# Optimization experiments

Hardware: AMD Instinct MI355X
Metric: run time of the kernel (lower is better)

## Reference

```python
import jax, jax.numpy as jnp
import numpy as np

TAU = 0.07          # softmax temperature
THR = 0.3           # Jaccard similarity threshold for positive pairs
EPS_NORM = 1e-12    # F.normalize eps


def setup_inputs() -> dict:
    key = jax.random.key(0)
    k1, k2, k3 = jax.random.split(key, 3)
    N, D, A = 4096, 128, 512
    z1 = jax.random.normal(k1, (N, D), dtype=jnp.float32)
    z2 = jax.random.normal(k2, (N, D), dtype=jnp.float32)
    labels = jax.random.randint(k3, (N, A), 0, 2).astype(jnp.int32)
    return {"z1": z1, "z2": z2, "labels": labels}


def _l2_normalize(x):
    n = jnp.linalg.norm(x, axis=-1, keepdims=True)
    return x / jnp.maximum(n, EPS_NORM)


def reference(z1, z2, labels):
    # Implements the N > 1000 (chunked) branch of SupConLoss.forward,
    # vectorized over all anchors at once (chunking is just tiling; math identical).
    N = z1.shape[0]
    idx = jnp.arange(N)

    z1n = _l2_normalize(z1)                       # (N, D)
    z2n = _l2_normalize(z2)                       # (N, D)
    z_all = jnp.concatenate([z1n, z2n], axis=0)   # (2N, D)

    # Jaccard label similarity -> positive-pair mask
    lab = labels.astype(jnp.float32)              # (N, A)
    inter = lab @ lab.T                           # (N, N)
    s = lab.sum(axis=1, keepdims=True)            # (N, 1)
    union = s + s.T - inter
    jaccard = inter / (union + 1e-8)
    pos_label = jaccard >= THR                    # (N, N) bool

    # pos mask over 2N columns: label-positives in both halves,
    # augmented view [j, N+j] forced True, self column [j, j] forced False.
    pos_mask = jnp.concatenate([pos_label, pos_label], axis=1)  # (N, 2N)
    pos_mask = pos_mask.at[idx, N + idx].set(True)
    pos_mask = pos_mask.at[idx, idx].set(False)

    # similarity of z1 anchors against all 2N embeddings
    sim = (z1n @ z_all.T) / TAU                   # (N, 2N)
    sim = sim - jax.lax.stop_gradient(sim.max(axis=1, keepdims=True))
    exp_sim = jnp.exp(sim)

    # denominator excludes the self column [j, j]
    denom = exp_sim.sum(axis=1, keepdims=True) - exp_sim[idx, idx][:, None]
    log_prob = sim - jnp.log(denom + 1e-8)

    num_pos = jnp.maximum(pos_mask.sum(axis=1), 1)
    loss_per_sample = -jnp.where(pos_mask, log_prob, 0.0).sum(axis=1) / num_pos
    return loss_per_sample.sum() / N
```

## Files before the change

kernel.cpp:

```cpp
#include <hip/hip_runtime.h>
#include <math.h>

#define N_ROWS 4096
#define DIM    128
#define A_LAB  512
#define INV_TAU 14.285714285714286f

typedef __attribute__((ext_vector_type(8))) short short8;
typedef __attribute__((ext_vector_type(4))) float f32x4;
typedef __attribute__((ext_vector_type(4))) int i32x4;
typedef __attribute__((ext_vector_type(16))) int i32x16;


__device__ __forceinline__ unsigned short f2bf(float f) {
  unsigned int u = __builtin_bit_cast(unsigned int, f);
  u += 0x7fffu + ((u >> 16) & 1u);
  return (unsigned short)(u >> 16);
}

__device__ __forceinline__ void gl_lds16(const void* g, void* l) {
  __builtin_amdgcn_global_load_lds(
      (const __attribute__((address_space(1))) unsigned int*)g,
      (__attribute__((address_space(3))) unsigned int*)l, 16, 0, 0);
}

__global__ __launch_bounds__(256) void k_norm_pack(
    const float* __restrict__ z1, const float* __restrict__ z2,
    const int* __restrict__ labels,
    unsigned int* __restrict__ zbf, uint2* __restrict__ labs8,
    int* __restrict__ s, float* __restrict__ out)
{
  if (blockIdx.x == 0 && threadIdx.x == 0) out[0] = 0.0f;
  const int wave = threadIdx.x >> 6, lane = threadIdx.x & 63;
  const int r = blockIdx.x * 4 + wave;
  const float* src = (r < N_ROWS) ? (z1 + (size_t)r * DIM)
                                  : (z2 + (size_t)(r - N_ROWS) * DIM);
  float2 x = ((const float2*)src)[lane];
  float ss = x.x * x.x + x.y * x.y;
  #pragma unroll
  for (int off = 32; off > 0; off >>= 1) ss += __shfl_xor(ss, off);
  const float inv = 1.0f / fmaxf(sqrtf(ss), 1e-12f);
  const unsigned int lo = f2bf(x.x * inv);
  const unsigned int hi = f2bf(x.y * inv);
  {
    const int U  = lane >> 2;
    const int Up = U ^ (r & 15);
    zbf[(size_t)r * 64 + Up * 4 + (lane & 3)] = (hi << 16) | lo;
  }

  if (r < N_ROWS) {
    const int4* lp = (const int4*)(labels + (size_t)r * A_LAB);
    const int4 a = lp[2 * lane], b = lp[2 * lane + 1];
    const unsigned int w0 = (unsigned int)(a.x != 0)       | ((unsigned int)(a.y != 0) << 8)
                          | ((unsigned int)(a.z != 0) << 16) | ((unsigned int)(a.w != 0) << 24);
    const unsigned int w1 = (unsigned int)(b.x != 0)       | ((unsigned int)(b.y != 0) << 8)
                          | ((unsigned int)(b.z != 0) << 16) | ((unsigned int)(b.w != 0) << 24);
    uint2 v; v.x = w0; v.y = w1;
    const int Ul  = lane >> 1;
    const int cc  = Ul >> 3, uu = Ul & 7;
    const int Ulp = (cc << 3) | (uu ^ (r & 7));
    labs8[(size_t)r * 64 + Ulp * 2 + (lane & 1)] = v;
    int cnt = __popc(w0) + __popc(w1);
    #pragma unroll
    for (int off = 32; off > 0; off >>= 1) cnt += __shfl_xor(cnt, off);
    if (lane == 0) s[r] = cnt;
  }
}

__global__ __launch_bounds__(256, 2) void k_jac(
    const unsigned char* __restrict__ labs8, const int* __restrict__ s,
    unsigned int* __restrict__ pm)
{
  __shared__ uint4 lds[4096];
  const int tid = threadIdx.x;
  const int ibase = blockIdx.x * 128, jbase = blockIdx.y * 128;
  const int wave = tid >> 6, lane = tid & 63;
  const int wrow = (wave >> 1) * 64, wcol = (wave & 1) * 64;
  const int col = lane & 31, h = lane >> 5;

  const int s3i = 3 * s[ibase + wrow + lane];
  const int s3j = 3 * s[jbase + wcol + lane];

  #pragma unroll
  for (int it = 0; it < 4; ++it) {
    const int g = wave * 256 + it * 64 + lane;
    const int r = g >> 3, u = g & 7;
    gl_lds16(labs8 + (((size_t)(ibase + r)) << 9) + u * 16,
             &lds[wave * 256 + it * 64]);
    gl_lds16(labs8 + (((size_t)(jbase + r)) << 9) + u * 16,
             &lds[1024 + wave * 256 + it * 64]);
  }
  __syncthreads();

  i32x16 acc[2][2];
  #pragma unroll
  for (int rt = 0; rt < 2; ++rt)
    #pragma unroll
    for (int nt = 0; nt < 2; ++nt)
      #pragma unroll
      for (int e = 0; e < 16; ++e) acc[rt][nt][e] = 0;

  for (int ck = 0; ck < 4; ++ck) {
    const int cur = (ck & 1) * 2048;
    if (ck < 3) {
      const int nxt = ((ck + 1) & 1) * 2048;
      #pragma unroll
      for (int it = 0; it < 4; ++it) {
        const int g = wave * 256 + it * 64 + lane;
        const int r = g >> 3, u = g & 7;
        const size_t go = (size_t)(ck + 1) * 128 + u * 16;
        gl_lds16(labs8 + (((size_t)(ibase + r)) << 9) + go,
                 &lds[nxt + wave * 256 + it * 64]);
        gl_lds16(labs8 + (((size_t)(jbase + r)) << 9) + go,
                 &lds[nxt + 1024 + wave * 256 + it * 64]);
      }
    }
    #pragma unroll
    for (int ks = 0; ks < 4; ++ks) {
      const int u = ks * 2 + h;
      i32x4 a[2], b[2];
      #pragma unroll
      for (int rt = 0; rt < 2; ++rt) {
        const int m = wrow + rt * 32 + col;
        a[rt] = *(const i32x4*)&lds[cur + m * 8 + (u ^ (m & 7))];
      }
      #pragma unroll
      for (int nt = 0; nt < 2; ++nt) {
        const int m = wcol + nt * 32 + col;
        b[nt] = *(const i32x4*)&lds[cur + 1024 + m * 8 + (u ^ (m & 7))];
      }
      #pragma unroll
      for (int rt = 0; rt < 2; ++rt)
        #pragma unroll
        for (int nt = 0; nt < 2; ++nt)
          acc[rt][nt] = __builtin_amdgcn_mfma_i32_32x32x32_i8(a[rt], b[nt], acc[rt][nt], 0, 0, 0);
    }
    if (ck < 3) __syncthreads();
  }

  #pragma unroll
  for (int rt = 0; rt < 2; ++rt)
    #pragma unroll
    for (int nt = 0; nt < 2; ++nt) {
      const int w = (jbase + wcol + nt * 32) >> 5;
      const int sj = __shfl(s3j, nt * 32 + col);
      #pragma unroll
      for (int reg = 0; reg < 16; ++reg) {
        const int r0 = (reg & 3) + 8 * (reg >> 2);
        const int si = __shfl(s3i, rt * 32 + r0 + 4 * h);
        const bool pred = 13 * acc[rt][nt][reg] >= si + sj;
        const unsigned long long bal = __ballot(pred);
        const int i0 = ibase + wrow + rt * 32 + r0;
        if (lane == 0)      pm[(size_t)i0 * 128 + w]       = (unsigned int)bal;
        else if (lane == 1) pm[(size_t)(i0 + 4) * 128 + w] = (unsigned int)(bal >> 32);
      }
    }
}

__global__ __launch_bounds__(256, 2) void k_main(
    const unsigned short* __restrict__ zbf, const unsigned int* __restrict__ pm,
    float* __restrict__ part)
{
  __shared__ unsigned short lds[2 * 128 * 128];
  uint4* sU = (uint4*)lds;
  const int tid = threadIdx.x;
  const int abase = blockIdx.x * 128;
  const int cbase = blockIdx.y * 128;
  const int wave = tid >> 6, lane = tid & 63;

  {
    const char* gz = (const char*)zbf;
    #pragma unroll
    for (int it = 0; it < 8; ++it) {
      const int g = wave * 512 + it * 64 + lane;
      const int r = g >> 4, u = g & 15;
      gl_lds16(gz + (size_t)(abase + r) * 256 + u * 16, &sU[wave * 512 + it * 64]);
      gl_lds16(gz + (size_t)(cbase + r) * 256 + u * 16, &sU[2048 + wave * 512 + it * 64]);
    }
  }
  __syncthreads();

  const int col = lane & 15, quad = lane >> 4;
  const int wrow = wave * 32;
  const uint4* sAu = sU;
  const uint4* sBu = sU + 2048;

  short8 afr[2][4];
  #pragma unroll
  for (int rt = 0; rt < 2; ++rt)
    #pragma unroll
    for (int kf = 0; kf < 4; ++kf) {
      const int r = wrow + rt * 16 + col;
      const int u = kf * 4 + quad;
      afr[rt][kf] = *(const short8*)&sAu[r * 16 + (u ^ (r & 15))];
    }

  f32x4 acc[2][8];
  #pragma unroll
  for (int rt = 0; rt < 2; ++rt)
    #pragma unroll
    for (int nt = 0; nt < 8; ++nt) acc[rt][nt] = (f32x4){0, 0, 0, 0};

  #pragma unroll
  for (int nt = 0; nt < 8; ++nt) {
    short8 bfr[4];
    #pragma unroll
    for (int kf = 0; kf < 4; ++kf) {
      const int r = nt * 16 + col;
      const int u = kf * 4 + quad;
      bfr[kf] = *(const short8*)&sBu[r * 16 + (u ^ (r & 15))];
    }
    #pragma unroll
    for (int rt = 0; rt < 2; ++rt)
      #pragma unroll
      for (int kf = 0; kf < 4; ++kf)
        acc[rt][nt] = __builtin_amdgcn_mfma_f32_16x16x32_bf16(
            afr[rt][kf], bfr[kf], acc[rt][nt], 0, 0, 0);
  }

  const bool left = (cbase < N_ROWS);
  const int cw0 = (cbase & (N_ROWS - 1)) >> 5;
  float lacc[2][4], Sacc[2][4], Pcnt[2][4];
  #pragma unroll
  for (int rt = 0; rt < 2; ++rt)
    #pragma unroll
    for (int reg = 0; reg < 4; ++reg) { lacc[rt][reg] = 0; Sacc[rt][reg] = 0; Pcnt[rt][reg] = 0; }

  #pragma unroll
  for (int rt = 0; rt < 2; ++rt) {
    unsigned int pw[4][4];
    #pragma unroll
    for (int reg = 0; reg < 4; ++reg) {
      const int i = abase + wrow + rt * 16 + quad * 4 + reg;
      #pragma unroll
      for (int w = 0; w < 4; ++w) pw[reg][w] = pm[(size_t)i * 128 + cw0 + w];
    }
    #pragma unroll
    for (int nt = 0; nt < 8; ++nt) {
      const int j = cbase + nt * 16 + col;
      const int jc = j & (N_ROWS - 1);
      const int bitpos = jc & 31;
      const int w = nt >> 1;
      #pragma unroll
      for (int reg = 0; reg < 4; ++reg) {
        const int i = abase + wrow + rt * 16 + quad * 4 + reg;
        const float d = acc[rt][nt][reg];
        const bool bit = (pw[reg][w] >> bitpos) & 1;
        const bool self = left && (j == i);
        const bool pos = left ? (bit && !self) : (bit || (jc == i));
        const float e = __expf((d - 1.0f) * INV_TAU);
        if (!self) lacc[rt][reg] += e;
        if (pos) { Sacc[rt][reg] += d; Pcnt[rt][reg] += 1.0f; }
      }
    }
  }

  #pragma unroll
  for (int rt = 0; rt < 2; ++rt)
    #pragma unroll
    for (int reg = 0; reg < 4; ++reg) {
      float l = lacc[rt][reg], S = Sacc[rt][reg], P = Pcnt[rt][reg];
      #pragma unroll
      for (int m = 1; m < 16; m <<= 1) {
        l += __shfl_xor(l, m);
        S += __shfl_xor(S, m);
        P += __shfl_xor(P, m);
      }
      if (col == 0) {
        const int i = abase + wrow + rt * 16 + quad * 4 + reg;
        float* base = part + (size_t)blockIdx.y * 3 * 4096;
        base[i] = l;
        base[4096 + i] = S;
        base[8192 + i] = P;
      }
    }
}

__global__ __launch_bounds__(128) void k_loss(
    const float* __restrict__ part, float* __restrict__ out)
{
  const int a = blockIdx.x * 128 + threadIdx.x;
  float l = 0.0f, S = 0.0f, P = 0.0f;
  #pragma unroll 8
  for (int by = 0; by < 64; ++by) {
    const float* b = part + (size_t)by * 3 * 4096;
    l += b[a];
    S += b[4096 + a];
    P += b[8192 + a];
  }
  const float np = fmaxf(P, 1.0f);
  float v = INV_TAU + logf(l + 1e-8f) - (S * INV_TAU) / np;
  #pragma unroll
  for (int off = 32; off > 0; off >>= 1) v += __shfl_xor(v, off);
  __shared__ float ws2[2];
  const int wave = threadIdx.x >> 6, lane = threadIdx.x & 63;
  if (lane == 0) ws2[wave] = v;
  __syncthreads();
  if (threadIdx.x == 0) atomicAdd(out, (ws2[0] + ws2[1]) * (1.0f / (float)N_ROWS));
}

extern "C" void kernel_launch(void* const* d_in, const int* in_sizes, int n_in,
                              void* d_out, int out_size, void* d_ws, size_t ws_size,
                              hipStream_t stream) {
  const float* z1 = (const float*)d_in[0];
  const float* z2 = (const float*)d_in[1];
  const int* labels = (const int*)d_in[2];
  float* out = (float*)d_out;
  char* ws = (char*)d_ws;

  unsigned int* zbf    = (unsigned int*)(ws);
  uint2* labs8         = (uint2*)(ws + 2097152);
  int* s               = (int*)(ws + 4194304);
  unsigned int* pm     = (unsigned int*)(ws + 4210688);
  float* part          = (float*)(ws + 6307840);

  hipLaunchKernelGGL(k_norm_pack, dim3(2048), dim3(256), 0, stream,
                     z1, z2, labels, zbf, labs8, s, out);
  hipLaunchKernelGGL(k_jac, dim3(32, 32), dim3(256), 0, stream,
                     (const unsigned char*)labs8, s, pm);
  hipLaunchKernelGGL(k_main, dim3(32, 64), dim3(256), 0, stream,
                     (const unsigned short*)zbf, pm, part);
  hipLaunchKernelGGL(k_loss, dim3(32), dim3(128), 0, stream, part, out);
}
```

Before: 128.3 us.

## Fuse Jaccard mask and similarity kernels, keep positive mask in LDS

Merges the Jaccard mask kernel and the similarity/softmax kernel into one kernel per 128x128 tile. The positive-pair bitmask now lives in shared memory instead of a global round trip, and each block handles both the z1 and z2 column halves in sequence, reloading the B tile between them. Per-block partial sums are combined with float atomics into a single buffer zeroed in the pack kernel, so the final loss kernel no longer loops over 64 partial slices. This removes one launch and the global mask traffic, at the cost of longer blocks, extra barriers, atomic contention, and nondeterministic summation order.

```diff
diff --git a/kernel.cpp b/kernel.cpp
--- a/kernel.cpp
+++ b/kernel.cpp
@@ -28,9 +28,13 @@
     const float* __restrict__ z1, const float* __restrict__ z2,
     const int* __restrict__ labels,
     unsigned int* __restrict__ zbf, uint2* __restrict__ labs8,
-    int* __restrict__ s, float* __restrict__ out)
+    int* __restrict__ s, float* __restrict__ part, float* __restrict__ out)
 {
-  if (blockIdx.x == 0 && threadIdx.x == 0) out[0] = 0.0f;
+  {
+    const int idx = blockIdx.x * 256 + threadIdx.x;
+    if (idx < 3 * 4096) part[idx] = 0.0f;
+    if (idx == 0) out[0] = 0.0f;
+  }
   const int wave = threadIdx.x >> 6, lane = threadIdx.x & 63;
   const int r = blockIdx.x * 4 + wave;
   const float* src = (r < N_ROWS) ? (z1 + (size_t)r * DIM)
@@ -67,19 +71,21 @@
   }
 }
 
-__global__ __launch_bounds__(256, 2) void k_jac(
+__global__ __launch_bounds__(256, 2) void k_fused(
     const unsigned char* __restrict__ labs8, const int* __restrict__ s,
-    unsigned int* __restrict__ pm)
+    const unsigned short* __restrict__ zbf, float* __restrict__ part)
 {
   __shared__ uint4 lds[4096];
+  __shared__ unsigned int pmL[128 * 4];
   const int tid = threadIdx.x;
   const int ibase = blockIdx.x * 128, jbase = blockIdx.y * 128;
   const int wave = tid >> 6, lane = tid & 63;
-  const int wrow = (wave >> 1) * 64, wcol = (wave & 1) * 64;
-  const int col = lane & 31, h = lane >> 5;
-
-  const int s3i = 3 * s[ibase + wrow + lane];
-  const int s3j = 3 * s[jbase + wcol + lane];
+
+  const int jwr = (wave >> 1) * 64, jwc = (wave & 1) * 64;
+  const int col32 = lane & 31, h = lane >> 5;
+
+  const int s3i = 3 * s[ibase + jwr + lane];
+  const int s3j = 3 * s[jbase + jwc + lane];
 
   #pragma unroll
   for (int it = 0; it < 4; ++it) {
@@ -92,13 +98,13 @@
   }
   __syncthreads();
 
-  i32x16 acc[2][2];
+  i32x16 jacc[2][2];
   #pragma unroll
   for (int rt = 0; rt < 2; ++rt)
     #pragma unroll
     for (int nt = 0; nt < 2; ++nt)
       #pragma unroll
-      for (int e = 0; e < 16; ++e) acc[rt][nt][e] = 0;
+      for (int e = 0; e < 16; ++e) jacc[rt][nt][e] = 0;
 
   for (int ck = 0; ck < 4; ++ck) {
     const int cur = (ck & 1) * 2048;
@@ -121,138 +127,144 @@
       i32x4 a[2], b[2];
       #pragma unroll
       for (int rt = 0; rt < 2; ++rt) {
-        const int m = wrow + rt * 32 + col;
+        const int m = jwr + rt * 32 + col32;
         a[rt] = *(const i32x4*)&lds[cur + m * 8 + (u ^ (m & 7))];
       }
       #pragma unroll
       for (int nt = 0; nt < 2; ++nt) {
-        const int m = wcol + nt * 32 + col;
+        const int m = jwc + nt * 32 + col32;
         b[nt] = *(const i32x4*)&lds[cur + 1024 + m * 8 + (u ^ (m & 7))];
       }
       #pragma unroll
       for (int rt = 0; rt < 2; ++rt)
         #pragma unroll
         for (int nt = 0; nt < 2; ++nt)
-          acc[rt][nt] = __builtin_amdgcn_mfma_i32_32x32x32_i8(a[rt], b[nt], acc[rt][nt], 0, 0, 0);
+          jacc[rt][nt] = __builtin_amdgcn_mfma_i32_32x32x32_i8(a[rt], b[nt], jacc[rt][nt], 0, 0, 0);
     }
     if (ck < 3) __syncthreads();
   }
 
+  __syncthreads();
+
+  {
+    const char* gz = (const char*)zbf;
+    #pragma unroll
+    for (int it = 0; it < 8; ++it) {
+      const int g = wave * 512 + it * 64 + lane;
+      const int r = g >> 4, u = g & 15;
+      gl_lds16(gz + (size_t)(ibase + r) * 256 + u * 16, &lds[wave * 512 + it * 64]);
+      gl_lds16(gz + (size_t)(jbase + r) * 256 + u * 16, &lds[2048 + wave * 512 + it * 64]);
+    }
+  }
+
   #pragma unroll
   for (int rt = 0; rt < 2; ++rt)
     #pragma unroll
     for (int nt = 0; nt < 2; ++nt) {
-      const int w = (jbase + wcol + nt * 32) >> 5;
-      const int sj = __shfl(s3j, nt * 32 + col);
+      const int wl = (jwc >> 5) + nt;
+      const int sj = __shfl(s3j, nt * 32 + col32);
       #pragma unroll
       for (int reg = 0; reg < 16; ++reg) {
         const int r0 = (reg & 3) + 8 * (reg >> 2);
         const int si = __shfl(s3i, rt * 32 + r0 + 4 * h);
-        const bool pred = 13 * acc[rt][nt][reg] >= si + sj;
+        const bool pred = 13 * jacc[rt][nt][reg] >= si + sj;
         const unsigned long long bal = __ballot(pred);
-        const int i0 = ibase + wrow + rt * 32 + r0;
-        if (lane == 0)      pm[(size_t)i0 * 128 + w]       = (unsigned int)bal;
-        else if (lane == 1) pm[(size_t)(i0 + 4) * 128 + w] = (unsigned int)(bal >> 32);
-      }
-    }
-}
-
-__global__ __launch_bounds__(256, 2) void k_main(
-    const unsigned short* __restrict__ zbf, const unsigned int* __restrict__ pm,
-    float* __restrict__ part)
-{
-  __shared__ unsigned short lds[2 * 128 * 128];
-  uint4* sU = (uint4*)lds;
-  const int tid = threadIdx.x;
-  const int abase = blockIdx.x * 128;
-  const int cbase = blockIdx.y * 128;
-  const int wave = tid >> 6, lane = tid & 63;
-
-  {
-    const char* gz = (const char*)zbf;
-    #pragma unroll
-    for (int it = 0; it < 8; ++it) {
-      const int g = wave * 512 + it * 64 + lane;
-      const int r = g >> 4, u = g & 15;
-      gl_lds16(gz + (size_t)(abase + r) * 256 + u * 16, &sU[wave * 512 + it * 64]);
-      gl_lds16(gz + (size_t)(cbase + r) * 256 + u * 16, &sU[2048 + wave * 512 + it * 64]);
-    }
-  }
+        const int lr = jwr + rt * 32 + r0;
+        if (lane == 0)      pmL[lr * 4 + wl]       = (unsigned int)bal;
+        else if (lane == 1) pmL[(lr + 4) * 4 + wl] = (unsigned int)(bal >> 32);
+      }
+    }
+
   __syncthreads();
 
   const int col = lane & 15, quad = lane >> 4;
-  const int wrow = wave * 32;
-  const uint4* sAu = sU;
-  const uint4* sBu = sU + 2048;
+  const int swr = wave * 32;
+  const uint4* sAu = lds;
+  const uint4* sBu = lds + 2048;
 
   short8 afr[2][4];
   #pragma unroll
   for (int rt = 0; rt < 2; ++rt)
     #pragma unroll
     for (int kf = 0; kf < 4; ++kf) {
-      const int r = wrow + rt * 16 + col;
+      const int r = swr + rt * 16 + col;
       const int u = kf * 4 + quad;
       afr[rt][kf] = *(const short8*)&sAu[r * 16 + (u ^ (r & 15))];
     }
 
-  f32x4 acc[2][8];
-  #pragma unroll
-  for (int rt = 0; rt < 2; ++rt)
-    #pragma unroll
-    for (int nt = 0; nt < 8; ++nt) acc[rt][nt] = (f32x4){0, 0, 0, 0};
-
-  #pragma unroll
-  for (int nt = 0; nt < 8; ++nt) {
-    short8 bfr[4];
-    #pragma unroll
-    for (int kf = 0; kf < 4; ++kf) {
-      const int r = nt * 16 + col;
-      const int u = kf * 4 + quad;
-      bfr[kf] = *(const short8*)&sBu[r * 16 + (u ^ (r & 15))];
-    }
+  float lacc[2][4], Sacc[2][4], Pcnt[2][4];
+  #pragma unroll
+  for (int rt = 0; rt < 2; ++rt)
+    #pragma unroll
+    for (int reg = 0; reg < 4; ++reg) { lacc[rt][reg] = 0; Sacc[rt][reg] = 0; Pcnt[rt][reg] = 0; }
+
+  #pragma unroll
+  for (int half = 0; half < 2; ++half) {
+    f32x4 acc[2][8];
     #pragma unroll
     for (int rt = 0; rt < 2; ++rt)
       #pragma unroll
-      for (int kf = 0; kf < 4; ++kf)
-        acc[rt][nt] = __builtin_amdgcn_mfma_f32_16x16x32_bf16(
-            afr[rt][kf], bfr[kf], acc[rt][nt], 0, 0, 0);
-  }
-
-  const bool left = (cbase < N_ROWS);
-  const int cw0 = (cbase & (N_ROWS - 1)) >> 5;
-  float lacc[2][4], Sacc[2][4], Pcnt[2][4];
-  #pragma unroll
-  for (int rt = 0; rt < 2; ++rt)
-    #pragma unroll
-    for (int reg = 0; reg < 4; ++reg) { lacc[rt][reg] = 0; Sacc[rt][reg] = 0; Pcnt[rt][reg] = 0; }
-
-  #pragma unroll
-  for (int rt = 0; rt < 2; ++rt) {
-    unsigned int pw[4][4];
-    #pragma unroll
-    for (int reg = 0; reg < 4; ++reg) {
-      const int i = abase + wrow + rt * 16 + quad * 4 + reg;
-      #pragma unroll
-      for (int w = 0; w < 4; ++w) pw[reg][w] = pm[(size_t)i * 128 + cw0 + w];
-    }
+      for (int nt = 0; nt < 8; ++nt) acc[rt][nt] = (f32x4){0, 0, 0, 0};
+
     #pragma unroll
     for (int nt = 0; nt < 8; ++nt) {
-      const int j = cbase + nt * 16 + col;
-      const int jc = j & (N_ROWS - 1);
-      const int bitpos = jc & 31;
-      const int w = nt >> 1;
+      short8 bfr[4];
+      #pragma unroll
+      for (int kf = 0; kf < 4; ++kf) {
+        const int r = nt * 16 + col;
+        const int u = kf * 4 + quad;
+        bfr[kf] = *(const short8*)&sBu[r * 16 + (u ^ (r & 15))];
+      }
+      #pragma unroll
+      for (int rt = 0; rt < 2; ++rt)
+        #pragma unroll
+        for (int kf = 0; kf < 4; ++kf)
+          acc[rt][nt] = __builtin_amdgcn_mfma_f32_16x16x32_bf16(
+              afr[rt][kf], bfr[kf], acc[rt][nt], 0, 0, 0);
+    }
+
+    if (half == 0) {
+      __syncthreads();
+      const char* gz = (const char*)zbf;
+      #pragma unroll
+      for (int it = 0; it < 8; ++it) {
+        const int g = wave * 512 + it * 64 + lane;
+        const int r = g >> 4, u = g & 15;
+        gl_lds16(gz + (size_t)(N_ROWS + jbase + r) * 256 + u * 16,
+                 &lds[2048 + wave * 512 + it * 64]);
+      }
+    }
+
+    const bool left = (half == 0);
+    #pragma unroll
+    for (int rt = 0; rt < 2; ++rt) {
+      unsigned int pw[4][4];
       #pragma unroll
       for (int reg = 0; reg < 4; ++reg) {
-        const int i = abase + wrow + rt * 16 + quad * 4 + reg;
-        const float d = acc[rt][nt][reg];
-        const bool bit = (pw[reg][w] >> bitpos) & 1;
-        const bool self = left && (j == i);
-        const bool pos = left ? (bit && !self) : (bit || (jc == i));
-        const float e = __expf((d - 1.0f) * INV_TAU);
-        if (!self) lacc[rt][reg] += e;
-        if (pos) { Sacc[rt][reg] += d; Pcnt[rt][reg] += 1.0f; }
-      }
-    }
+        const int li = swr + rt * 16 + quad * 4 + reg;
+        #pragma unroll
+        for (int w = 0; w < 4; ++w) pw[reg][w] = pmL[li * 4 + w];
+      }
+      #pragma unroll
+      for (int nt = 0; nt < 8; ++nt) {
+        const int joff = nt * 16 + col;
+        const int jc = jbase + joff;
+        const int bitpos = joff & 31;
+        const int w = nt >> 1;
+        #pragma unroll
+        for (int reg = 0; reg < 4; ++reg) {
+          const int i = ibase + swr + rt * 16 + quad * 4 + reg;
+          const float d = acc[rt][nt][reg];
+          const bool bit = (pw[reg][w] >> bitpos) & 1;
+          const bool self = left && (jc == i);
+          const bool pos = left ? (bit && !self) : (bit || (jc == i));
+          const float e = __expf((d - 1.0f) * INV_TAU);
+          if (!self) lacc[rt][reg] += e;
+          if (pos) { Sacc[rt][reg] += d; Pcnt[rt][reg] += 1.0f; }
+        }
+      }
+    }
+    if (half == 0) __syncthreads();
   }
 
   #pragma unroll
@@ -267,11 +279,10 @@
         P += __shfl_xor(P, m);
       }
       if (col == 0) {
-        const int i = abase + wrow + rt * 16 + quad * 4 + reg;
-        float* base = part + (size_t)blockIdx.y * 3 * 4096;
-        base[i] = l;
-        base[4096 + i] = S;
-        base[8192 + i] = P;
+        const int i = ibase + swr + rt * 16 + quad * 4 + reg;
+        atomicAdd(&part[i], l);
+        atomicAdd(&part[4096 + i], S);
+        atomicAdd(&part[8192 + i], P);
       }
     }
 }
@@ -280,14 +291,9 @@
     const float* __restrict__ part, float* __restrict__ out)
 {
   const int a = blockIdx.x * 128 + threadIdx.x;
-  float l = 0.0f, S = 0.0f, P = 0.0f;
-  #pragma unroll 8
-  for (int by = 0; by < 64; ++by) {
-    const float* b = part + (size_t)by * 3 * 4096;
-    l += b[a];
-    S += b[4096 + a];
-    P += b[8192 + a];
-  }
+  const float l = part[a];
+  const float S = part[4096 + a];
+  const float P = part[8192 + a];
   const float np = fmaxf(P, 1.0f);
   float v = INV_TAU + logf(l + 1e-8f) - (S * INV_TAU) / np;
   #pragma unroll
@@ -311,14 +317,11 @@
   unsigned int* zbf    = (unsigned int*)(ws);
   uint2* labs8         = (uint2*)(ws + 2097152);
   int* s               = (int*)(ws + 4194304);
-  unsigned int* pm     = (unsigned int*)(ws + 4210688);
-  float* part          = (float*)(ws + 6307840);
+  float* part          = (float*)(ws + 4210688);
 
   hipLaunchKernelGGL(k_norm_pack, dim3(2048), dim3(256), 0, stream,
-                     z1, z2, labels, zbf, labs8, s, out);
-  hipLaunchKernelGGL(k_jac, dim3(32, 32), dim3(256), 0, stream,
-                     (const unsigned char*)labs8, s, pm);
-  hipLaunchKernelGGL(k_main, dim3(32, 64), dim3(256), 0, stream,
-                     (const unsigned short*)zbf, pm, part);
+                     z1, z2, labels, zbf, labs8, s, part, out);
+  hipLaunchKernelGGL(k_fused, dim3(32, 32), dim3(256), 0, stream,
+                     (const unsigned char*)labs8, s, (const unsigned short*)zbf, part);
   hipLaunchKernelGGL(k_loss, dim3(32), dim3(128), 0, stream, part, out);
 }
```

Result: faster. 111.7 us (-12.9%).
